# Optimization experiments

Measured on AMD Instinct MI355X. Metric: run time of the kernel, lower is better.

The kernel has to match this reference:

```python
import jax, jax.numpy as jnp
import numpy as np

H = 1024          # hidden_size
NH = 16           # num_attention_heads
HD = H // NH      # attention_head_size = 64
B, S = 8, 1024
LN_EPS = 1e-12


def setup_inputs() -> dict:
    key = jax.random.key(0)
    ks = jax.random.split(key, 12)
    sc = 0.02
    return {
        "input_tensor": jax.random.normal(ks[0], (B, S, H), dtype=jnp.float32),
        "attention_mask": jnp.zeros((B, S), dtype=jnp.float32),
        # LinearMem params (quantization disabled -> plain Linear, torch layout [out,in])
        "Wq": jax.random.normal(ks[1], (H, H), dtype=jnp.float32) * sc,
        "bq": jnp.zeros((H,), dtype=jnp.float32),
        "Wk": jax.random.normal(ks[2], (H, H), dtype=jnp.float32) * sc,
        "bk": jnp.zeros((H,), dtype=jnp.float32),
        "Wv": jax.random.normal(ks[3], (H, H), dtype=jnp.float32) * sc,
        "bv": jnp.zeros((H,), dtype=jnp.float32),
        "Wo": jax.random.normal(ks[4], (H, H), dtype=jnp.float32) * sc,
        "bo": jnp.zeros((H,), dtype=jnp.float32),
        "ln_gamma": jnp.ones((H,), dtype=jnp.float32),
        "ln_beta": jnp.zeros((H,), dtype=jnp.float32),
    }


def _heads(x):  # [B,S,H] -> [B,NH,S,HD]
    return x.reshape(B, S, NH, HD).transpose(0, 2, 1, 3)


def reference(input_tensor, attention_mask, Wq, bq, Wk, bk, Wv, bv, Wo, bo, ln_gamma, ln_beta):
    # Q/K/V projections (LinearMem with quantization disabled == Linear)
    q = _heads(jnp.einsum('bsh,oh->bso', input_tensor, Wq) + bq)
    k = _heads(jnp.einsum('bsh,oh->bso', input_tensor, Wk) + bk)
    v = _heads(jnp.einsum('bsh,oh->bso', input_tensor, Wv) + bv)
    scores = jnp.einsum('bnqd,bnkd->bnqk', q, k) / np.float32(np.sqrt(HD))
    scores = scores + attention_mask[:, None, None, :]  # additive mask [B,1,1,S]
    probs = jax.nn.softmax(scores, axis=-1)  # dropout = identity in eval
    ctx = jnp.einsum('bnqk,bnkd->bnqd', probs, v)
    ctx = ctx.transpose(0, 2, 1, 3).reshape(B, S, H)
    # output projection + residual LayerNorm (eps=1e-12)
    out = jnp.einsum('bsh,oh->bso', ctx, Wo) + bo
    resid = out + input_tensor
    mu = jnp.mean(resid, axis=-1, keepdims=True)
    var = jnp.mean(jnp.square(resid - mu), axis=-1, keepdims=True)
    return (resid - mu) * jax.lax.rsqrt(var + LN_EPS) * ln_gamma + ln_beta
```

## Files before the change

kernel.cpp:

```cpp
#include <hip/hip_runtime.h>

#define NHh 16

typedef unsigned short ushortT;
typedef __attribute__((ext_vector_type(8))) short short8;
typedef __attribute__((ext_vector_type(4))) float floatx4;

__device__ __forceinline__ ushortT f2bf(float x) {
    union { float f; unsigned int u; } cv; cv.f = x;
    unsigned int u = cv.u;
    unsigned int r = u + 0x7fffu + ((u >> 16) & 1u);
    return (ushortT)(r >> 16);
}

__device__ __forceinline__ unsigned pack2_trunc(float a, float b) {
    union { float f; unsigned u; } ua, ub;
    ua.f = a; ub.f = b;
    return (ub.u & 0xffff0000u) | (ua.u >> 16);
}

__device__ __forceinline__ void gload_lds16(const ushortT* g, ushortT* l) {
    __builtin_amdgcn_global_load_lds(
        (const __attribute__((address_space(1))) void*)g,
        (__attribute__((address_space(3))) void*)l, 16, 0, 0);
}

__global__ __launch_bounds__(256) void cvt_all(const float* __restrict__ x,
        const float* __restrict__ W0, const float* __restrict__ W1,
        const float* __restrict__ W2, const float* __restrict__ W3,
        ushortT* __restrict__ Xb, ushortT* __restrict__ Wall, ushortT* __restrict__ Wob) {
    int bid = blockIdx.x;
    const float* in; ushortT* out; int i;
    if (bid < 8192) {
        in = x; out = Xb; i = bid * 256 + threadIdx.x;
    } else {
        int z = (bid - 8192) >> 10;
        in = (z == 0) ? W0 : (z == 1) ? W1 : (z == 2) ? W2 : W3;
        out = (z < 3) ? (Wall + (size_t)z * 1048576) : Wob;
        i = ((bid - 8192) & 1023) * 256 + threadIdx.x;
    }
    float4 f = ((const float4*)in)[i];
    uint2 o;
    o.x = (unsigned)f2bf(f.x) | ((unsigned)f2bf(f.y) << 16);
    o.y = (unsigned)f2bf(f.z) | ((unsigned)f2bf(f.w) << 16);
    ((uint2*)out)[i] = o;
}

__global__ __launch_bounds__(1024, 4) void qkv16(
        const ushortT* __restrict__ X, const ushortT* __restrict__ Wall,
        const float* __restrict__ b0, const float* __restrict__ b1, const float* __restrict__ b2,
        ushortT* __restrict__ Qo, ushortT* __restrict__ Ko, ushortT* __restrict__ Vo) {
    __shared__ __align__(16) ushortT As[2 * 16384];
    __shared__ __align__(16) ushortT Bs[2 * 12288];

    const int l = blockIdx.x;
    const int xcd = l & 7;
    const int j = l >> 3;
    const int mg = j >> 4;
    const int nt = j & 15;
    const int arow0 = (mg * 8 + xcd) * 256;
    const int brow0 = nt * 192;

    const int tid = threadIdx.x;
    const int lane = tid & 63;
    const int w = tid >> 6;
    const int wr = w >> 2;
    const int wc = w & 3;
    const int qd = lane >> 4, ln = lane & 15;

    const ushortT* srcA[2]; int oA[2];
#pragma unroll
    for (int k = 0; k < 2; k++) {
        int o = k * 16384 + tid * 16;
        int rowblk = o >> 11, ks = (o >> 10) & 1, r = (o >> 6) & 15;
        int c2 = ((o >> 4) & 3) ^ ((r >> 3) << 1);
        srcA[k] = X + (size_t)(arow0 + rowblk * 16 + r) * 1024 + ks * 32 + c2 * 8;
        oA[k] = o;
    }
    const ushortT* srcB[2]; int oB[2];
#pragma unroll
    for (int k = 0; k < 2; k++) {
        int o = k * 16384 + tid * 16;
        int rowblk = o >> 11, ks = (o >> 10) & 1, r = (o >> 6) & 15;
        int c2 = ((o >> 4) & 3) ^ ((r >> 3) << 1);
        srcB[k] = Wall + (size_t)(brow0 + rowblk * 16 + r) * 1024 + ks * 32 + c2 * 8;
        oB[k] = o;
    }

    floatx4 acc[4][3];
#pragma unroll
    for (int i = 0; i < 4; i++)
#pragma unroll
        for (int jj = 0; jj < 3; jj++) acc[i][jj] = (floatx4){0.f, 0.f, 0.f, 0.f};

    auto STAGE = [&](int buf) {
#pragma unroll
        for (int k = 0; k < 2; k++) {
            gload_lds16(srcA[k], (ushortT*)((char*)As + buf * 32768 + oA[k]));
            srcA[k] += 64;
        }
        gload_lds16(srcB[0], (ushortT*)((char*)Bs + buf * 24576 + oB[0]));
        srcB[0] += 64;
        if (tid < 512) {
            gload_lds16(srcB[1], (ushortT*)((char*)Bs + buf * 24576 + oB[1]));
            srcB[1] += 64;
        }
    };

    const int lnc = ln * 64 + ((qd ^ ((ln >> 3) << 1)) * 16);

    STAGE(0);
    asm volatile("s_waitcnt vmcnt(0)" ::: "memory");
    __builtin_amdgcn_s_barrier();

    for (int T = 0; T < 16; T++) {
        const char* Ab = (const char*)As + (T & 1) * 32768;
        const char* Bb = (const char*)Bs + (T & 1) * 24576;
        if (T < 15) STAGE((T + 1) & 1);
        short8 af[4], bf[3];
#pragma unroll
        for (int ks = 0; ks < 2; ks++) {
#pragma unroll
            for (int mi = 0; mi < 4; mi++)
                af[mi] = *(const short8*)(Ab + (wr * 4 + mi) * 2048 + ks * 1024 + lnc);
#pragma unroll
            for (int ni = 0; ni < 3; ni++)
                bf[ni] = *(const short8*)(Bb + (wc * 3 + ni) * 2048 + ks * 1024 + lnc);
            asm volatile("s_waitcnt lgkmcnt(0)" ::: "memory");
            __builtin_amdgcn_sched_barrier(0);
            __builtin_amdgcn_s_setprio(1);
#pragma unroll
            for (int mi = 0; mi < 4; mi++)
#pragma unroll
                for (int ni = 0; ni < 3; ni++)
                    acc[mi][ni] = __builtin_amdgcn_mfma_f32_16x16x32_bf16(af[mi], bf[ni], acc[mi][ni], 0, 0, 0);
            __builtin_amdgcn_s_setprio(0);
        }
        asm volatile("s_waitcnt vmcnt(0)" ::: "memory");
        __builtin_amdgcn_s_barrier();
    }

#pragma unroll
    for (int ni = 0; ni < 3; ni++) {
        int n = brow0 + wc * 48 + ni * 16 + ln;
        int z = n >> 10;
        int col = n & 1023;
        int h = col >> 6, d = col & 63;
        const float* bias = (z == 0) ? b0 : (z == 1) ? b1 : b2;
        float bb = bias[col];
        if (z == 2) {
#pragma unroll
            for (int mi = 0; mi < 4; mi++) {
                int m = arow0 + wr * 64 + mi * 16 + qd * 4;
                int b = m >> 10, s = m & 1023;
                ushort4 pk;
                pk.x = f2bf(acc[mi][ni][0] + bb);
                pk.y = f2bf(acc[mi][ni][1] + bb);
                pk.z = f2bf(acc[mi][ni][2] + bb);
                pk.w = f2bf(acc[mi][ni][3] + bb);
                *(ushort4*)&Vo[((size_t)(b * NHh + h) * 64 + d) * 1024 + s] = pk;
            }
        } else {
            ushortT* Out = z ? Ko : Qo;
#pragma unroll
            for (int mi = 0; mi < 4; mi++) {
#pragma unroll
                for (int r2 = 0; r2 < 4; r2++) {
                    int m = arow0 + wr * 64 + mi * 16 + qd * 4 + r2;
                    int b = m >> 10, s = m & 1023;
                    Out[(size_t)((b * NHh + h) * 1024 + s) * 64 + d] =
                        f2bf(acc[mi][ni][r2] + bb);
                }
            }
        }
    }
}

__global__ __launch_bounds__(1024, 4) void oproj16(const ushortT* __restrict__ A,
        const ushortT* __restrict__ Wt, const float* __restrict__ bias,
        const float* __restrict__ Xf, float* __restrict__ Pj) {
    __shared__ __align__(16) ushortT As[2 * 16384];
    __shared__ __align__(16) ushortT Bs[2 * 8192];

    const int l = blockIdx.x;
    const int xcd = l & 7;
    const int j = l >> 3;
    const int tid = threadIdx.x;
    const int lane = tid & 63;
    const int w = tid >> 6;
    const int wr = w >> 2, wc = w & 3;
    const int qd = lane >> 4, ln = lane & 15;

    const int arow0 = ((j & 3) * 8 + xcd) * 256;
    const int brow0 = (j >> 2) * 128;

    const ushortT* srcA[2]; int oA[2];
#pragma unroll
    for (int k = 0; k < 2; k++) {
        int o = k * 16384 + tid * 16;
        int rowblk = o >> 11, ks = (o >> 10) & 1, r = (o >> 6) & 15;
        int c2 = ((o >> 4) & 3) ^ ((r >> 3) << 1);
        srcA[k] = A + (size_t)(arow0 + rowblk * 16 + r) * 1024 + ks * 32 + c2 * 8;
        oA[k] = o;
    }
    const ushortT* srcB0; int oB0;
    {
        int o = tid * 16;
        int rowblk = o >> 11, ks = (o >> 10) & 1, r = (o >> 6) & 15;
        int c2 = ((o >> 4) & 3) ^ ((r >> 3) << 1);
        srcB0 = Wt + (size_t)(brow0 + rowblk * 16 + r) * 1024 + ks * 32 + c2 * 8;
        oB0 = o;
    }

    floatx4 acc[4][2];
#pragma unroll
    for (int i = 0; i < 4; i++)
#pragma unroll
        for (int jj = 0; jj < 2; jj++) acc[i][jj] = (floatx4){0.f, 0.f, 0.f, 0.f};

    auto STAGE = [&](int buf) {
#pragma unroll
        for (int k = 0; k < 2; k++) {
            gload_lds16(srcA[k], (ushortT*)((char*)As + buf * 32768 + oA[k]));
            srcA[k] += 64;
        }
        gload_lds16(srcB0, (ushortT*)((char*)Bs + buf * 16384 + oB0));
        srcB0 += 64;
    };

    const int lnc = ln * 64 + ((qd ^ ((ln >> 3) << 1)) * 16);

    STAGE(0);
    asm volatile("s_waitcnt vmcnt(0)" ::: "memory");
    __builtin_amdgcn_s_barrier();

    for (int T = 0; T < 16; T++) {
        const char* Ab = (const char*)As + (T & 1) * 32768;
        const char* Bb = (const char*)Bs + (T & 1) * 16384;
        if (T < 15) STAGE((T + 1) & 1);
        short8 af[4], bf[2];
#pragma unroll
        for (int ks = 0; ks < 2; ks++) {
#pragma unroll
            for (int mi = 0; mi < 4; mi++)
                af[mi] = *(const short8*)(Ab + (wr * 4 + mi) * 2048 + ks * 1024 + lnc);
#pragma unroll
            for (int ni = 0; ni < 2; ni++)
                bf[ni] = *(const short8*)(Bb + (wc * 2 + ni) * 2048 + ks * 1024 + lnc);
            asm volatile("s_waitcnt lgkmcnt(0)" ::: "memory");
            __builtin_amdgcn_sched_barrier(0);
            __builtin_amdgcn_s_setprio(1);
#pragma unroll
            for (int mi = 0; mi < 4; mi++)
#pragma unroll
                for (int ni = 0; ni < 2; ni++)
                    acc[mi][ni] = __builtin_amdgcn_mfma_f32_16x16x32_bf16(af[mi], bf[ni], acc[mi][ni], 0, 0, 0);
            __builtin_amdgcn_s_setprio(0);
        }
        asm volatile("s_waitcnt vmcnt(0)" ::: "memory");
        __builtin_amdgcn_s_barrier();
    }

#pragma unroll
    for (int ni = 0; ni < 2; ni++) {
        int n = brow0 + wc * 32 + ni * 16 + ln;
        float bb = bias[n];
#pragma unroll
        for (int mi = 0; mi < 4; mi++) {
#pragma unroll
            for (int r2 = 0; r2 < 4; r2++) {
                int m = arow0 + wr * 64 + mi * 16 + qd * 4 + r2;
                Pj[(size_t)m * 1024 + n] = acc[mi][ni][r2] + bb + Xf[(size_t)m * 1024 + n];
            }
        }
    }
}

__global__ __launch_bounds__(512, 4) void attn8(const ushortT* __restrict__ Q,
        const ushortT* __restrict__ K, const ushortT* __restrict__ Vg_t,
        const float* __restrict__ mask, ushortT* __restrict__ ctx) {
    __shared__ __align__(16) ushortT Ks[128 * 64];
    __shared__ __align__(16) ushortT Vt[64 * 128];
    __shared__ __align__(16) ushortT Ps[8][32 * 36];

    const int tid = threadIdx.x;
    const int lane = tid & 63;
    const int w = tid >> 6;
    const int qd = lane >> 4;
    const int ln = lane & 15;
    const int l = blockIdx.x;
    const int bh = l & 127;
    const int b = bh >> 4;
    const int h = bh & 15;
    const int qb = l >> 7;

    const ushortT* Qg = Q + (size_t)bh * 65536;
    const ushortT* Kg = K + (size_t)bh * 65536;
    const ushortT* Vg = Vg_t + (size_t)bh * 65536;
    const float* mrow = mask + b * 1024;
    const float LOG2E = 1.4426950408889634f;
    const float SCL = 0.125f * 1.4426950408889634f;

    short8 qf[2][2];
#pragma unroll
    for (int g = 0; g < 2; g++)
#pragma unroll
        for (int ks = 0; ks < 2; ks++)
            qf[g][ks] = *(const short8*)(Qg + (size_t)(qb * 256 + w * 32 + g * 16 + ln) * 64 + ks * 32 + qd * 8);

    float lst[2] = {0.f, 0.f};
    floatx4 accO[2][4];
#pragma unroll
    for (int g = 0; g < 2; g++)
#pragma unroll
        for (int j = 0; j < 4; j++) accO[g][j] = (floatx4){0.f, 0.f, 0.f, 0.f};

    const int ksr = lane >> 3;
    const int kc  = lane & 7;
    const int vdr = lane >> 4;
    const int vcc = lane & 15;

    for (int kt = 0; kt < 8; ++kt) {
        __syncthreads();

#pragma unroll
        for (int ii = 0; ii < 2; ii++) {
            int i = w * 2 + ii;
            int srow = i * 8 + ksr;
            gload_lds16(Kg + (size_t)(kt * 128 + srow) * 64 + (kc ^ ksr) * 8,
                        Ks + i * 512 + lane * 8);
        }
#pragma unroll
        for (int ii = 0; ii < 2; ii++) {
            int i = w * 2 + ii;
            int d = i * 4 + vdr;
            gload_lds16(Vg + (size_t)d * 1024 + kt * 128 + (vcc ^ (d & 15)) * 8,
                        Vt + i * 512 + lane * 8);
        }

        __syncthreads();

#pragma unroll
        for (int h2 = 0; h2 < 2; ++h2) {
#pragma unroll
            for (int mip = 0; mip < 2; ++mip) {
                floatx4 sv[2][2];
#pragma unroll
                for (int mi2 = 0; mi2 < 2; mi2++)
#pragma unroll
                    for (int g = 0; g < 2; g++) sv[mi2][g] = (floatx4){0.f, 0.f, 0.f, 0.f};
#pragma unroll
                for (int ks = 0; ks < 2; ks++) {
                    short8 af[2];
#pragma unroll
                    for (int mi2 = 0; mi2 < 2; mi2++)
                        af[mi2] = *(const short8*)&Ks[(h2 * 64 + mip * 32 + mi2 * 16 + ln) * 64 +
                                                      (((ks * 4 + qd) ^ (ln & 7)) * 8)];
#pragma unroll
                    for (int mi2 = 0; mi2 < 2; mi2++)
#pragma unroll
                        for (int g = 0; g < 2; g++)
                            sv[mi2][g] = __builtin_amdgcn_mfma_f32_16x16x32_bf16(af[mi2], qf[g][ks], sv[mi2][g], 0, 0, 0);
                }

#pragma unroll
                for (int mi2 = 0; mi2 < 2; mi2++) {
                    floatx4 m4 = *(const floatx4*)(mrow + kt * 128 + h2 * 64 + mip * 32 + mi2 * 16 + qd * 4);
                    floatx4 mm;
                    mm[0] = m4[0] * LOG2E; mm[1] = m4[1] * LOG2E;
                    mm[2] = m4[2] * LOG2E; mm[3] = m4[3] * LOG2E;
#pragma unroll
                    for (int g = 0; g < 2; g++) {
                        float p0 = __builtin_amdgcn_exp2f(sv[mi2][g][0] * SCL + mm[0]);
                        float p1 = __builtin_amdgcn_exp2f(sv[mi2][g][1] * SCL + mm[1]);
                        float p2 = __builtin_amdgcn_exp2f(sv[mi2][g][2] * SCL + mm[2]);
                        float p3 = __builtin_amdgcn_exp2f(sv[mi2][g][3] * SCL + mm[3]);
                        lst[g] += (p0 + p1) + (p2 + p3);
                        uint2 wv;
                        wv.x = pack2_trunc(p0, p1);
                        wv.y = pack2_trunc(p2, p3);
                        *(uint2*)&Ps[w][(g * 16 + ln) * 36 + mi2 * 16 + qd * 4] = wv;
                    }
                }

                short8 ap[2], bv[4];
#pragma unroll
                for (int g = 0; g < 2; g++)
                    ap[g] = *(const short8*)&Ps[w][(g * 16 + ln) * 36 + qd * 8];
#pragma unroll
                for (int j = 0; j < 4; j++)
                    bv[j] = *(const short8*)&Vt[(j * 16 + ln) * 128 +
                                                (((h2 * 8 + mip * 4 + qd) ^ ln) * 8)];
#pragma unroll
                for (int g = 0; g < 2; g++)
#pragma unroll
                    for (int j = 0; j < 4; j++)
                        accO[g][j] = __builtin_amdgcn_mfma_f32_16x16x32_bf16(ap[g], bv[j], accO[g][j], 0, 0, 0);
            }
        }
    }

#pragma unroll
    for (int g = 0; g < 2; g++) {
        lst[g] += __shfl_xor(lst[g], 16, 64);
        lst[g] += __shfl_xor(lst[g], 32, 64);
    }

#pragma unroll
    for (int g = 0; g < 2; g++) {
#pragma unroll
        for (int r = 0; r < 4; r++) {
            float lv = __shfl(lst[g], qd * 4 + r, 64);
            float linv = 1.f / lv;
            int q = qb * 256 + w * 32 + g * 16 + qd * 4 + r;
#pragma unroll
            for (int j = 0; j < 4; j++) {
                int d = j * 16 + ln;
                ctx[((size_t)(b * 1024 + q)) * 1024 + h * 64 + d] = f2bf(accO[g][j][r] * linv);
            }
        }
    }
}

__global__ __launch_bounds__(256) void ln_res(const float* __restrict__ Pj,
        const float* __restrict__ gamma, const float* __restrict__ beta, float* __restrict__ out) {
    __shared__ float red[8];
    int row = blockIdx.x;
    int t = threadIdx.x;
    const float4 p4 = ((const float4*)(Pj + (size_t)row * 1024))[t];
    float r0 = p4.x, r1 = p4.y, r2 = p4.z, r3 = p4.w;
    float s = r0 + r1 + r2 + r3;
    float ss = r0 * r0 + r1 * r1 + r2 * r2 + r3 * r3;
#pragma unroll
    for (int o = 1; o < 64; o <<= 1) { s += __shfl_xor(s, o, 64); ss += __shfl_xor(ss, o, 64); }
    int w = t >> 6;
    if ((t & 63) == 0) { red[w] = s; red[4 + w] = ss; }
    __syncthreads();
    s = red[0] + red[1] + red[2] + red[3];
    ss = red[4] + red[5] + red[6] + red[7];
    float mu = s * (1.f / 1024.f);
    float var = ss * (1.f / 1024.f) - mu * mu;
    float inv = rsqrtf(var + 1e-12f);
    const float4 g4 = ((const float4*)gamma)[t];
    const float4 b4 = ((const float4*)beta)[t];
    float4 o4;
    o4.x = (r0 - mu) * inv * g4.x + b4.x;
    o4.y = (r1 - mu) * inv * g4.y + b4.y;
    o4.z = (r2 - mu) * inv * g4.z + b4.z;
    o4.w = (r3 - mu) * inv * g4.w + b4.w;
    ((float4*)(out + (size_t)row * 1024))[t] = o4;
}

extern "C" void kernel_launch(void* const* d_in, const int* in_sizes, int n_in,
                              void* d_out, int out_size, void* d_ws, size_t ws_size,
                              hipStream_t stream) {
    const float* x     = (const float*)d_in[0];
    const float* mask  = (const float*)d_in[1];
    const float* Wq    = (const float*)d_in[2];
    const float* bq    = (const float*)d_in[3];
    const float* Wk    = (const float*)d_in[4];
    const float* bk    = (const float*)d_in[5];
    const float* Wv    = (const float*)d_in[6];
    const float* bv    = (const float*)d_in[7];
    const float* Wo    = (const float*)d_in[8];
    const float* bo    = (const float*)d_in[9];
    const float* gamma = (const float*)d_in[10];
    const float* beta  = (const float*)d_in[11];
    float* out = (float*)d_out;

    char* ws = (char*)d_ws;
    ushortT* Xb   = (ushortT*)(ws);
    ushortT* Wall = (ushortT*)(ws + (16u << 20));
    ushortT* Wob  = (ushortT*)(ws + (22u << 20));
    ushortT* Qb   = (ushortT*)(ws + (24u << 20));
    ushortT* Kb   = (ushortT*)(ws + (40u << 20));
    ushortT* Vb   = (ushortT*)(ws + (56u << 20));
    ushortT* Cb   = (ushortT*)(ws);
    float*   Pj   = (float*)(ws + (24u << 20));

    cvt_all<<<12288, 256, 0, stream>>>(x, Wq, Wk, Wv, Wo, Xb, Wall, Wob);
    qkv16<<<512, 1024, 0, stream>>>(Xb, Wall, bq, bk, bv, Qb, Kb, Vb);
    attn8<<<512, 512, 0, stream>>>(Qb, Kb, Vb, mask, Cb);
    oproj16<<<256, 1024, 0, stream>>>(Cb, Wob, bo, x, Pj);
    ln_res<<<8192, 256, 0, stream>>>(Pj, gamma, beta, out);
}
```

Measured before the change: 264.4 us.

## Software-pipeline LDS fragment reads against MFMAs in the QKV and output GEMMs

Restructures the main loop of both projection GEMMs so fragments for the next k-substep are read from LDS into a second register set while the MFMAs for the current substep run. Two tiles are staged up front, and the next global-to-LDS stage is issued right after the barrier into the buffer just consumed. The goal is to hide LDS read latency and global load latency behind matrix math instead of waiting on lgkmcnt before every MFMA block. The cost is extra VGPRs for the doubled fragment registers, which could pressure occupancy at the given launch bounds, plus more complex waitcnt ordering.

```diff
diff --git a/kernel.cpp b/kernel.cpp
--- a/kernel.cpp
+++ b/kernel.cpp
@@ -109,35 +109,51 @@
 
     const int lnc = ln * 64 + ((qd ^ ((ln >> 3) << 1)) * 16);
 
-    STAGE(0);
-    asm volatile("s_waitcnt vmcnt(0)" ::: "memory");
+    short8 a0[4], bf0[3], a1[4], bf1[3];
+
+    auto RD = [&](short8 (&af)[4], short8 (&bf)[3], const char* Ab, const char* Bb, int ksb) {
+#pragma unroll
+        for (int mi = 0; mi < 4; mi++)
+            af[mi] = *(const short8*)(Ab + (wr * 4 + mi) * 2048 + ksb + lnc);
+#pragma unroll
+        for (int ni = 0; ni < 3; ni++)
+            bf[ni] = *(const short8*)(Bb + (wc * 3 + ni) * 2048 + ksb + lnc);
+    };
+    auto MM = [&](short8 (&af)[4], short8 (&bf)[3]) {
+        __builtin_amdgcn_s_setprio(1);
+#pragma unroll
+        for (int mi = 0; mi < 4; mi++)
+#pragma unroll
+            for (int ni = 0; ni < 3; ni++)
+                acc[mi][ni] = __builtin_amdgcn_mfma_f32_16x16x32_bf16(af[mi], bf[ni], acc[mi][ni], 0, 0, 0);
+        __builtin_amdgcn_s_setprio(0);
+    };
+
+    STAGE(0); STAGE(1);
+    asm volatile("s_waitcnt vmcnt(3)" ::: "memory");
     __builtin_amdgcn_s_barrier();
+    RD(a0, bf0, (const char*)As, (const char*)Bs, 0);
+    asm volatile("s_waitcnt lgkmcnt(0)" ::: "memory");
+    __builtin_amdgcn_sched_barrier(0);
 
     for (int T = 0; T < 16; T++) {
         const char* Ab = (const char*)As + (T & 1) * 32768;
         const char* Bb = (const char*)Bs + (T & 1) * 24576;
-        if (T < 15) STAGE((T + 1) & 1);
-        short8 af[4], bf[3];
-#pragma unroll
-        for (int ks = 0; ks < 2; ks++) {
-#pragma unroll
-            for (int mi = 0; mi < 4; mi++)
-                af[mi] = *(const short8*)(Ab + (wr * 4 + mi) * 2048 + ks * 1024 + lnc);
-#pragma unroll
-            for (int ni = 0; ni < 3; ni++)
-                bf[ni] = *(const short8*)(Bb + (wc * 3 + ni) * 2048 + ks * 1024 + lnc);
-            asm volatile("s_waitcnt lgkmcnt(0)" ::: "memory");
-            __builtin_amdgcn_sched_barrier(0);
-            __builtin_amdgcn_s_setprio(1);
-#pragma unroll
-            for (int mi = 0; mi < 4; mi++)
-#pragma unroll
-                for (int ni = 0; ni < 3; ni++)
-                    acc[mi][ni] = __builtin_amdgcn_mfma_f32_16x16x32_bf16(af[mi], bf[ni], acc[mi][ni], 0, 0, 0);
-            __builtin_amdgcn_s_setprio(0);
-        }
+        const char* An = (const char*)As + ((T + 1) & 1) * 32768;
+        const char* Bn = (const char*)Bs + ((T + 1) & 1) * 24576;
+        RD(a1, bf1, Ab, Bb, 1024);
+        __builtin_amdgcn_sched_barrier(0);
+        MM(a0, bf0);
+        asm volatile("s_waitcnt lgkmcnt(0)" ::: "memory");
         asm volatile("s_waitcnt vmcnt(0)" ::: "memory");
+        __builtin_amdgcn_sched_barrier(0);
         __builtin_amdgcn_s_barrier();
+        if (T < 14) STAGE(T & 1);
+        if (T < 15) RD(a0, bf0, An, Bn, 0);
+        __builtin_amdgcn_sched_barrier(0);
+        MM(a1, bf1);
+        asm volatile("s_waitcnt lgkmcnt(0)" ::: "memory");
+        __builtin_amdgcn_sched_barrier(0);
     }
 
 #pragma unroll
@@ -230,35 +246,51 @@
 
     const int lnc = ln * 64 + ((qd ^ ((ln >> 3) << 1)) * 16);
 
-    STAGE(0);
-    asm volatile("s_waitcnt vmcnt(0)" ::: "memory");
+    short8 a0[4], bf0[2], a1[4], bf1[2];
+
+    auto RD = [&](short8 (&af)[4], short8 (&bf)[2], const char* Ab, const char* Bb, int ksb) {
+#pragma unroll
+        for (int mi = 0; mi < 4; mi++)
+            af[mi] = *(const short8*)(Ab + (wr * 4 + mi) * 2048 + ksb + lnc);
+#pragma unroll
+        for (int ni = 0; ni < 2; ni++)
+            bf[ni] = *(const short8*)(Bb + (wc * 2 + ni) * 2048 + ksb + lnc);
+    };
+    auto MM = [&](short8 (&af)[4], short8 (&bf)[2]) {
+        __builtin_amdgcn_s_setprio(1);
+#pragma unroll
+        for (int mi = 0; mi < 4; mi++)
+#pragma unroll
+            for (int ni = 0; ni < 2; ni++)
+                acc[mi][ni] = __builtin_amdgcn_mfma_f32_16x16x32_bf16(af[mi], bf[ni], acc[mi][ni], 0, 0, 0);
+        __builtin_amdgcn_s_setprio(0);
+    };
+
+    STAGE(0); STAGE(1);
+    asm volatile("s_waitcnt vmcnt(3)" ::: "memory");
     __builtin_amdgcn_s_barrier();
+    RD(a0, bf0, (const char*)As, (const char*)Bs, 0);
+    asm volatile("s_waitcnt lgkmcnt(0)" ::: "memory");
+    __builtin_amdgcn_sched_barrier(0);
 
     for (int T = 0; T < 16; T++) {
         const char* Ab = (const char*)As + (T & 1) * 32768;
         const char* Bb = (const char*)Bs + (T & 1) * 16384;
-        if (T < 15) STAGE((T + 1) & 1);
-        short8 af[4], bf[2];
-#pragma unroll
-        for (int ks = 0; ks < 2; ks++) {
-#pragma unroll
-            for (int mi = 0; mi < 4; mi++)
-                af[mi] = *(const short8*)(Ab + (wr * 4 + mi) * 2048 + ks * 1024 + lnc);
-#pragma unroll
-            for (int ni = 0; ni < 2; ni++)
-                bf[ni] = *(const short8*)(Bb + (wc * 2 + ni) * 2048 + ks * 1024 + lnc);
-            asm volatile("s_waitcnt lgkmcnt(0)" ::: "memory");
-            __builtin_amdgcn_sched_barrier(0);
-            __builtin_amdgcn_s_setprio(1);
-#pragma unroll
-            for (int mi = 0; mi < 4; mi++)
-#pragma unroll
-                for (int ni = 0; ni < 2; ni++)
-                    acc[mi][ni] = __builtin_amdgcn_mfma_f32_16x16x32_bf16(af[mi], bf[ni], acc[mi][ni], 0, 0, 0);
-            __builtin_amdgcn_s_setprio(0);
-        }
+        const char* An = (const char*)As + ((T + 1) & 1) * 32768;
+        const char* Bn = (const char*)Bs + ((T + 1) & 1) * 16384;
+        RD(a1, bf1, Ab, Bb, 1024);
+        __builtin_amdgcn_sched_barrier(0);
+        MM(a0, bf0);
+        asm volatile("s_waitcnt lgkmcnt(0)" ::: "memory");
         asm volatile("s_waitcnt vmcnt(0)" ::: "memory");
+        __builtin_amdgcn_sched_barrier(0);
         __builtin_amdgcn_s_barrier();
+        if (T < 14) STAGE(T & 1);
+        if (T < 15) RD(a0, bf0, An, Bn, 0);
+        __builtin_amdgcn_sched_barrier(0);
+        MM(a1, bf1);
+        asm volatile("s_waitcnt lgkmcnt(0)" ::: "memory");
+        __builtin_amdgcn_sched_barrier(0);
     }
 
 #pragma unroll
```

New measurement: 259.0 us. 2.0% less time.

## Keep softmax probabilities in registers and halve query rows per attention block

Applied to the files above, without the earlier changes.

The attention kernel drops the per-warp LDS staging of probabilities. The score MFMA output layout is now fed straight into a 16x16x16 bf16 MFMA against V, with a matching swizzled V column offset. Each warp now handles 16 query rows instead of 32, so the grid doubles to 1024 blocks and launch bounds ask for 8 waves per SIMD. This removes LDS write/read traffic and shrinks the register footprint for higher occupancy. In exchange, each K/V tile loaded into LDS serves half as many queries, so K/V reload traffic doubles, and the narrower MFMA issues more instructions per FLOP.

```diff
diff --git a/kernel.cpp b/kernel.cpp
--- a/kernel.cpp
+++ b/kernel.cpp
@@ -4,6 +4,7 @@
 
 typedef unsigned short ushortT;
 typedef __attribute__((ext_vector_type(8))) short short8;
+typedef __attribute__((ext_vector_type(4))) short short4v;
 typedef __attribute__((ext_vector_type(4))) float floatx4;
 
 __device__ __forceinline__ ushortT f2bf(float x) {
@@ -17,6 +18,17 @@
     union { float f; unsigned u; } ua, ub;
     ua.f = a; ub.f = b;
     return (ub.u & 0xffff0000u) | (ua.u >> 16);
+}
+
+__device__ __forceinline__ floatx4 mfma16(short4v a, short4v b, floatx4 c) {
+#if __has_builtin(__builtin_amdgcn_mfma_f32_16x16x16_bf16)
+    return __builtin_amdgcn_mfma_f32_16x16x16_bf16(a, b, c, 0, 0, 0);
+#elif __has_builtin(__builtin_amdgcn_mfma_f32_16x16x16bf16_1k)
+    return __builtin_amdgcn_mfma_f32_16x16x16bf16_1k(a, b, c, 0, 0, 0);
+#else
+    asm("v_mfma_f32_16x16x16_bf16 %0, %1, %2, %0" : "+v"(c) : "v"(a), "v"(b));
+    return c;
+#endif
 }
 
 __device__ __forceinline__ void gload_lds16(const ushortT* g, ushortT* l) {
@@ -276,12 +288,11 @@
     }
 }
 
-__global__ __launch_bounds__(512, 4) void attn8(const ushortT* __restrict__ Q,
+__global__ __launch_bounds__(512, 8) void attn16(const ushortT* __restrict__ Q,
         const ushortT* __restrict__ K, const ushortT* __restrict__ Vg_t,
         const float* __restrict__ mask, ushortT* __restrict__ ctx) {
     __shared__ __align__(16) ushortT Ks[128 * 64];
     __shared__ __align__(16) ushortT Vt[64 * 128];
-    __shared__ __align__(16) ushortT Ps[8][32 * 36];
 
     const int tid = threadIdx.x;
     const int lane = tid & 63;
@@ -301,19 +312,15 @@
     const float LOG2E = 1.4426950408889634f;
     const float SCL = 0.125f * 1.4426950408889634f;
 
-    short8 qf[2][2];
-#pragma unroll
-    for (int g = 0; g < 2; g++)
-#pragma unroll
-        for (int ks = 0; ks < 2; ks++)
-            qf[g][ks] = *(const short8*)(Qg + (size_t)(qb * 256 + w * 32 + g * 16 + ln) * 64 + ks * 32 + qd * 8);
-
-    float lst[2] = {0.f, 0.f};
-    floatx4 accO[2][4];
-#pragma unroll
-    for (int g = 0; g < 2; g++)
-#pragma unroll
-        for (int j = 0; j < 4; j++) accO[g][j] = (floatx4){0.f, 0.f, 0.f, 0.f};
+    short8 qf[2];
+#pragma unroll
+    for (int ks = 0; ks < 2; ks++)
+        qf[ks] = *(const short8*)(Qg + (size_t)(qb * 128 + w * 16 + ln) * 64 + ks * 32 + qd * 8);
+
+    float lst = 0.f;
+    floatx4 accO[4];
+#pragma unroll
+    for (int j = 0; j < 4; j++) accO[j] = (floatx4){0.f, 0.f, 0.f, 0.f};
 
     const int ksr = lane >> 3;
     const int kc  = lane & 7;
@@ -344,11 +351,9 @@
         for (int h2 = 0; h2 < 2; ++h2) {
 #pragma unroll
             for (int mip = 0; mip < 2; ++mip) {
-                floatx4 sv[2][2];
-#pragma unroll
-                for (int mi2 = 0; mi2 < 2; mi2++)
-#pragma unroll
-                    for (int g = 0; g < 2; g++) sv[mi2][g] = (floatx4){0.f, 0.f, 0.f, 0.f};
+                floatx4 sv[2];
+#pragma unroll
+                for (int mi2 = 0; mi2 < 2; mi2++) sv[mi2] = (floatx4){0.f, 0.f, 0.f, 0.f};
 #pragma unroll
                 for (int ks = 0; ks < 2; ks++) {
                     short8 af[2];
@@ -358,66 +363,43 @@
                                                       (((ks * 4 + qd) ^ (ln & 7)) * 8)];
 #pragma unroll
                     for (int mi2 = 0; mi2 < 2; mi2++)
-#pragma unroll
-                        for (int g = 0; g < 2; g++)
-                            sv[mi2][g] = __builtin_amdgcn_mfma_f32_16x16x32_bf16(af[mi2], qf[g][ks], sv[mi2][g], 0, 0, 0);
+                        sv[mi2] = __builtin_amdgcn_mfma_f32_16x16x32_bf16(af[mi2], qf[ks], sv[mi2], 0, 0, 0);
                 }
 
 #pragma unroll
                 for (int mi2 = 0; mi2 < 2; mi2++) {
                     floatx4 m4 = *(const floatx4*)(mrow + kt * 128 + h2 * 64 + mip * 32 + mi2 * 16 + qd * 4);
-                    floatx4 mm;
-                    mm[0] = m4[0] * LOG2E; mm[1] = m4[1] * LOG2E;
-                    mm[2] = m4[2] * LOG2E; mm[3] = m4[3] * LOG2E;
-#pragma unroll
-                    for (int g = 0; g < 2; g++) {
-                        float p0 = __builtin_amdgcn_exp2f(sv[mi2][g][0] * SCL + mm[0]);
-                        float p1 = __builtin_amdgcn_exp2f(sv[mi2][g][1] * SCL + mm[1]);
-                        float p2 = __builtin_amdgcn_exp2f(sv[mi2][g][2] * SCL + mm[2]);
-                        float p3 = __builtin_amdgcn_exp2f(sv[mi2][g][3] * SCL + mm[3]);
-                        lst[g] += (p0 + p1) + (p2 + p3);
-                        uint2 wv;
-                        wv.x = pack2_trunc(p0, p1);
-                        wv.y = pack2_trunc(p2, p3);
-                        *(uint2*)&Ps[w][(g * 16 + ln) * 36 + mi2 * 16 + qd * 4] = wv;
+                    float p0 = __builtin_amdgcn_exp2f(sv[mi2][0] * SCL + m4[0] * LOG2E);
+                    float p1 = __builtin_amdgcn_exp2f(sv[mi2][1] * SCL + m4[1] * LOG2E);
+                    float p2 = __builtin_amdgcn_exp2f(sv[mi2][2] * SCL + m4[2] * LOG2E);
+                    float p3 = __builtin_amdgcn_exp2f(sv[mi2][3] * SCL + m4[3] * LOG2E);
+                    lst += (p0 + p1) + (p2 + p3);
+                    union { unsigned u[2]; short4v s; } pk;
+                    pk.u[0] = pack2_trunc(p0, p1);
+                    pk.u[1] = pack2_trunc(p2, p3);
+                    const int cb = (((h2 * 8 + mip * 4 + mi2 * 2 + (qd >> 1)) ^ ln) * 8) + (qd & 1) * 4;
+#pragma unroll
+                    for (int j = 0; j < 4; j++) {
+                        short4v bv = *(const short4v*)&Vt[(j * 16 + ln) * 128 + cb];
+                        accO[j] = mfma16(pk.s, bv, accO[j]);
                     }
                 }
-
-                short8 ap[2], bv[4];
-#pragma unroll
-                for (int g = 0; g < 2; g++)
-                    ap[g] = *(const short8*)&Ps[w][(g * 16 + ln) * 36 + qd * 8];
-#pragma unroll
-                for (int j = 0; j < 4; j++)
-                    bv[j] = *(const short8*)&Vt[(j * 16 + ln) * 128 +
-                                                (((h2 * 8 + mip * 4 + qd) ^ ln) * 8)];
-#pragma unroll
-                for (int g = 0; g < 2; g++)
-#pragma unroll
-                    for (int j = 0; j < 4; j++)
-                        accO[g][j] = __builtin_amdgcn_mfma_f32_16x16x32_bf16(ap[g], bv[j], accO[g][j], 0, 0, 0);
             }
         }
     }
 
-#pragma unroll
-    for (int g = 0; g < 2; g++) {
-        lst[g] += __shfl_xor(lst[g], 16, 64);
-        lst[g] += __shfl_xor(lst[g], 32, 64);
-    }
-
-#pragma unroll
-    for (int g = 0; g < 2; g++) {
-#pragma unroll
-        for (int r = 0; r < 4; r++) {
-            float lv = __shfl(lst[g], qd * 4 + r, 64);
-            float linv = 1.f / lv;
-            int q = qb * 256 + w * 32 + g * 16 + qd * 4 + r;
-#pragma unroll
-            for (int j = 0; j < 4; j++) {
-                int d = j * 16 + ln;
-                ctx[((size_t)(b * 1024 + q)) * 1024 + h * 64 + d] = f2bf(accO[g][j][r] * linv);
-            }
+    lst += __shfl_xor(lst, 16, 64);
+    lst += __shfl_xor(lst, 32, 64);
+
+#pragma unroll
+    for (int r = 0; r < 4; r++) {
+        float lv = __shfl(lst, qd * 4 + r, 64);
+        float linv = 1.f / lv;
+        int q = qb * 128 + w * 16 + qd * 4 + r;
+#pragma unroll
+        for (int j = 0; j < 4; j++) {
+            int d = j * 16 + ln;
+            ctx[((size_t)(b * 1024 + q)) * 1024 + h * 64 + d] = f2bf(accO[j][r] * linv);
         }
     }
 }
@@ -480,7 +462,7 @@
 
     cvt_all<<<12288, 256, 0, stream>>>(x, Wq, Wk, Wv, Wo, Xb, Wall, Wob);
     qkv16<<<512, 1024, 0, stream>>>(Xb, Wall, bq, bk, bv, Qb, Kb, Vb);
-    attn8<<<512, 512, 0, stream>>>(Qb, Kb, Vb, mask, Cb);
+    attn16<<<1024, 512, 0, stream>>>(Qb, Kb, Vb, mask, Cb);
     oproj16<<<256, 1024, 0, stream>>>(Cb, Wob, bo, x, Pj);
     ln_res<<<8192, 256, 0, stream>>>(Pj, gamma, beta, out);
 }
```

New measurement: 290.1 us. +9.7%, slower.
